# Optimization experiments

Measured on AMD Instinct MI355X. Metric: run time of the kernel, lower is better.

The kernel has to match this reference:

```python
import jax, jax.numpy as jnp
import numpy as np

B, V, H = 4, 256, 128
EPS = 1e-5


def setup_inputs() -> dict:
    key = jax.random.key(0)
    ks = jax.random.split(key, 16)
    inp = {
        "h1": jax.random.normal(ks[0], (B, V, H), jnp.float32),
        "h2": jax.random.normal(ks[1], (B, V, H), jnp.float32),
        "e": jax.random.normal(ks[2], (B, V, V, H), jnp.float32),
        "graph": jax.random.randint(ks[3], (B, V, V), 0, 2, jnp.int32),
    }
    scale = 1.0 / np.sqrt(H)
    for i, nm in enumerate(["U1", "U2", "V1", "V2", "A1", "A2", "C"]):
        inp[f"W_{nm}"] = jax.random.normal(ks[4 + i], (H, H), jnp.float32) * scale
        inp[f"b_{nm}"] = jnp.zeros((H,), jnp.float32)
    for nm in ["h1", "h2", "e"]:
        inp[f"g_{nm}"] = jnp.ones((H,), jnp.float32)   # BN gamma
        inp[f"be_{nm}"] = jnp.zeros((H,), jnp.float32)  # BN beta
    return inp


def _lin(x, W, b):
    # torch nn.Linear: x @ W.T + b
    return jnp.einsum('...i,oi->...o', x, W) + b


def _bn(x, g, b):
    # BatchNorm1d with track_running_stats=False: batch stats over flattened leading dims
    sh = x.shape
    x2 = x.reshape(-1, sh[-1])
    m = x2.mean(axis=0)
    v = x2.var(axis=0)  # biased, as torch BN uses for normalization
    return ((x2 - m) * jax.lax.rsqrt(v + EPS) * g + b).reshape(sh)


def reference(h1, h2, e, graph,
              W_U1, b_U1, W_U2, b_U2, W_V1, b_V1, W_V2, b_V2,
              W_A1, b_A1, W_A2, b_A2, W_C, b_C,
              g_h1, be_h1, g_h2, be_h2, g_e, be_e):
    h1_in, h2_in, e_in = h1, h2, e

    Uh1 = _lin(h1, W_U1, b_U1)
    Uh2 = _lin(h2, W_U2, b_U2)
    Vh1 = _lin(h1, W_V1, b_V1)
    Vh2 = _lin(h2, W_V2, b_V2)

    # Wh1[b,i,j,h] = Vh1[b,j,h] + Vh2[b,i,h] ; Wh2 = transpose(1,2) pattern
    Wh1 = Vh1[:, None, :, :] + Vh2[:, :, None, :]
    Wh2 = Vh1[:, :, None, :] + Vh2[:, None, :, :]

    Ah1 = _lin(h1, W_A1, b_A1)
    Ah2 = _lin(h2, W_A2, b_A2)
    Ce = _lin(e, W_C, b_C)
    e_new = Ah1[:, None, :, :] + Ah2[:, :, None, :] + Ce  # B x V x V x H

    gates = jax.nn.sigmoid(e_new)
    gates_T = jax.nn.sigmoid(jnp.transpose(e_new, (0, 2, 1, 3)))

    # aggregation = 'sum' over dim 2 (graph unused for sum)
    h1n = Uh1 + jnp.sum(gates * Wh1, axis=2)
    h2n = Uh2 + jnp.sum(gates_T * Wh2, axis=2)

    h1n = jax.nn.relu(_bn(h1n, g_h1, be_h1))
    h2n = jax.nn.relu(_bn(h2n, g_h2, be_h2))
    e_out = jax.nn.relu(_bn(e_new, g_e, be_e))

    # mode == 'residual'
    return (h1_in + h1n, h2_in + h2n, e_in + e_out)
```

## Files before the change

### kernel.cpp

```cpp
#include <hip/hip_runtime.h>
#include <math.h>

#define BB 4
#define VV 256
#define HH 128
#define EPS 1e-5f

typedef __attribute__((ext_vector_type(8))) short short8;
typedef __attribute__((ext_vector_type(8))) __bf16 bf16x8;
typedef __attribute__((ext_vector_type(4))) float f32x4;

__device__ __forceinline__ float sigm_(float x) {
    return 1.0f / (1.0f + __expf(-x));
}

__device__ __forceinline__ bf16x8 as_bf(short8 s) {
    union { short8 s; bf16x8 b; } u; u.s = s; return u.b;
}

__device__ __forceinline__ void split8(const float4 x0, const float4 x1,
                                       short8& hi, short8& lo) {
    float xs[8] = {x0.x, x0.y, x0.z, x0.w, x1.x, x1.y, x1.z, x1.w};
    #pragma unroll
    for (int i = 0; i < 8; ++i) {
        unsigned u = __float_as_uint(xs[i]);
        unsigned hr = (u + 0x7fffu + ((u >> 16) & 1u)) & 0xffff0000u;
        hi[i] = (short)(hr >> 16);
        float r = xs[i] - __uint_as_float(hr);
        lo[i] = (short)(__float_as_uint(r) >> 16);
    }
}

__global__ __launch_bounds__(256) void k0_splitW(const float* __restrict__ W_C,
                                                 short* __restrict__ Whl) {
    int t = blockIdx.x * 256 + threadIdx.x;
    int lane = t & 63;
    int grp = t >> 6;
    int kstep = grp >> 3, nsub = grp & 7;
    int n = nsub * 16 + (lane & 15);
    int kb = kstep * 32 + ((lane >> 4) & 3) * 8;
    const float4* src = (const float4*)(W_C + (size_t)n * HH + kb);
    float4 x0 = src[0], x1 = src[1];
    short8 hi, lo;
    split8(x0, x1, hi, lo);
    short8* dst = (short8*)Whl;
    dst[(grp * 2 + 0) * 64 + lane] = hi;
    dst[(grp * 2 + 1) * 64 + lane] = lo;
}

struct LinArgs {
    const float* x1; const float* x2;
    const float* W[6]; const float* b[6];
    float* out[6];
};

__global__ __launch_bounds__(128) void k1_linears(LinArgs a) {
    __shared__ float xs[2][8][HH];
    const int t = threadIdx.x;
    const int r0 = blockIdx.x * 8;
    {
        const float4* s1 = (const float4*)(a.x1 + (size_t)r0 * HH);
        const float4* s2 = (const float4*)(a.x2 + (size_t)r0 * HH);
        float4* d1 = (float4*)&xs[0][0][0];
        float4* d2 = (float4*)&xs[1][0][0];
        #pragma unroll
        for (int p = 0; p < 2; ++p) {
            d1[t + p * 128] = s1[t + p * 128];
            d2[t + p * 128] = s2[t + p * 128];
        }
    }
    __syncthreads();
    const int h = t;
    for (int g = 0; g < 6; ++g) {
        const float* W = a.W[g];
        const float (*x)[HH] = (g < 3) ? xs[0] : xs[1];
        float acc[8];
        #pragma unroll
        for (int r = 0; r < 8; ++r) acc[r] = 0.f;
        const float4* Wrow = (const float4*)(W + (size_t)h * HH);
        #pragma unroll 8
        for (int kq = 0; kq < 32; ++kq) {
            float4 w4 = Wrow[kq];
            #pragma unroll
            for (int r = 0; r < 8; ++r) {
                float4 ev = *(const float4*)&x[r][kq * 4];
                acc[r] = fmaf(ev.x, w4.x, acc[r]);
                acc[r] = fmaf(ev.y, w4.y, acc[r]);
                acc[r] = fmaf(ev.z, w4.z, acc[r]);
                acc[r] = fmaf(ev.w, w4.w, acc[r]);
            }
        }
        float bias = a.b[g][h];
        float* O = a.out[g] + (size_t)r0 * HH + h;
        #pragma unroll
        for (int r = 0; r < 8; ++r) O[(size_t)r * HH] = acc[r] + bias;
    }
}

__global__ __launch_bounds__(512) void k2_main(
    const float* __restrict__ e,
    const short* __restrict__ Whl,
    const float* __restrict__ b_C,
    const float* __restrict__ A1, const float* __restrict__ A2,
    const float* __restrict__ V1, const float* __restrict__ V2,
    const float* __restrict__ U1,
    float* __restrict__ e_new,
    float* __restrict__ h1p,
    float* __restrict__ stats)
{
    __shared__ float red[8][3][8][16];
    const int t = threadIdx.x;
    const int l = t & 63;
    const int w = t >> 6;
    const int l15 = l & 15;
    const int lq = (l >> 4) & 3;
    const int bi = blockIdx.x;
    const int b = bi >> 8;

    const float* ebase = e + (size_t)bi * (VV * HH);
    const short8* Wf = (const short8*)Whl;

    f32x4 acc[2][8];
    #pragma unroll
    for (int js = 0; js < 2; ++js)
        #pragma unroll
        for (int ns = 0; ns < 8; ++ns)
            acc[js][ns] = (f32x4){0.f, 0.f, 0.f, 0.f};

    for (int kstep = 0; kstep < 4; ++kstep) {
        short8 bh[8], bl[8];
        #pragma unroll
        for (int ns = 0; ns < 8; ++ns) {
            int grp = kstep * 8 + ns;
            bh[ns] = Wf[(grp * 2 + 0) * 64 + l];
            bl[ns] = Wf[(grp * 2 + 1) * 64 + l];
        }
        short8 ah[2], al[2];
        #pragma unroll
        for (int js = 0; js < 2; ++js) {
            int row = w * 32 + js * 16 + l15;
            const float4* p = (const float4*)(ebase + (size_t)row * HH +
                                              kstep * 32 + lq * 8);
            float4 x0 = p[0], x1 = p[1];
            split8(x0, x1, ah[js], al[js]);
        }
        #pragma unroll
        for (int ns = 0; ns < 8; ++ns) {
            #pragma unroll
            for (int js = 0; js < 2; ++js) {
                acc[js][ns] = __builtin_amdgcn_mfma_f32_16x16x32_bf16(
                    as_bf(ah[js]), as_bf(bh[ns]), acc[js][ns], 0, 0, 0);
                acc[js][ns] = __builtin_amdgcn_mfma_f32_16x16x32_bf16(
                    as_bf(ah[js]), as_bf(bl[ns]), acc[js][ns], 0, 0, 0);
                acc[js][ns] = __builtin_amdgcn_mfma_f32_16x16x32_bf16(
                    as_bf(al[js]), as_bf(bh[ns]), acc[js][ns], 0, 0, 0);
            }
        }
    }

    float bCv[8], ah2v[8], vh2v[8];
    #pragma unroll
    for (int ns = 0; ns < 8; ++ns) {
        int n = ns * 16 + l15;
        bCv[ns]  = b_C[n];
        ah2v[ns] = A2[(size_t)bi * HH + n];
        vh2v[ns] = V2[(size_t)bi * HH + n];
    }
    float h1a[8], es[8], eq[8];
    #pragma unroll
    for (int ns = 0; ns < 8; ++ns) { h1a[ns] = 0.f; es[ns] = 0.f; eq[ns] = 0.f; }

    #pragma unroll
    for (int js = 0; js < 2; ++js) {
        #pragma unroll
        for (int r = 0; r < 4; ++r) {
            int j = w * 32 + js * 16 + lq * 4 + r;
            size_t base = (size_t)(b * VV + j) * HH;
            size_t obase = ((size_t)bi * VV + j) * HH;
            #pragma unroll
            for (int ns = 0; ns < 8; ++ns) {
                int n = ns * 16 + l15;
                float en = acc[js][ns][r] + bCv[ns] + A1[base + n] + ah2v[ns];
                e_new[obase + n] = en;
                float s = sigm_(en);
                h1a[ns] = fmaf(s, V1[base + n] + vh2v[ns], h1a[ns]);
                es[ns] += en;
                eq[ns] = fmaf(en, en, eq[ns]);
            }
        }
    }

    #pragma unroll
    for (int ns = 0; ns < 8; ++ns) {
        h1a[ns] += __shfl_xor(h1a[ns], 16);
        h1a[ns] += __shfl_xor(h1a[ns], 32);
        es[ns]  += __shfl_xor(es[ns], 16);
        es[ns]  += __shfl_xor(es[ns], 32);
        eq[ns]  += __shfl_xor(eq[ns], 16);
        eq[ns]  += __shfl_xor(eq[ns], 32);
    }
    if (l < 16) {
        #pragma unroll
        for (int ns = 0; ns < 8; ++ns) {
            red[w][0][ns][l15] = h1a[ns];
            red[w][1][ns][l15] = es[ns];
            red[w][2][ns][l15] = eq[ns];
        }
    }
    __syncthreads();
    if (t < 128) {
        int ns = t >> 4, li = t & 15;
        float h1t = 0.f, est = 0.f, eqt = 0.f;
        #pragma unroll
        for (int ww = 0; ww < 8; ++ww) {
            h1t += red[ww][0][ns][li];
            est += red[ww][1][ns][li];
            eqt += red[ww][2][ns][li];
        }
        int n = t;
        float pre = U1[(size_t)bi * HH + n] + h1t;
        h1p[(size_t)bi * HH + n] = pre;
        atomicAdd(&stats[0 * HH + n], est);
        atomicAdd(&stats[1 * HH + n], eqt);
        atomicAdd(&stats[2 * HH + n], pre);
        atomicAdd(&stats[3 * HH + n], pre * pre);
    }
}

__global__ __launch_bounds__(256) void k4_pass2(
    float* __restrict__ e_io,
    const float* __restrict__ e_in,
    const float* __restrict__ V1, const float* __restrict__ V2,
    const float* __restrict__ U2,
    const float* __restrict__ g_e, const float* __restrict__ be_e,
    float* __restrict__ h2p,
    float* __restrict__ stats)
{
    const int t = threadIdx.x;
    const int h = t & 127;
    const int jsub = t >> 7;
    const int blk = blockIdx.x;
    const int b = blk >> 7;
    const int J0 = (blk & 127) << 1;
    const int J = J0 + jsub;
    const int bJ = (b << 8) + J;

    const float inv_n = 1.0f / (float)(BB * VV * VV);
    float mean = stats[0 * HH + h] * inv_n;
    float var  = stats[1 * HH + h] * inv_n - mean * mean;
    float rstd = rsqrtf(var + EPS);
    float sc = rstd * g_e[h];
    float sh = be_e[h] - mean * sc;

    const float vh1 = V1[(size_t)bJ * HH + h];
    float h2acc = 0.f;

    #pragma unroll 8
    for (int I = 0; I < VV; ++I) {
        size_t off = ((size_t)((b * VV + I) * VV) + J0) * HH + t;
        float en = e_io[off];
        float s = sigm_(en);
        h2acc = fmaf(s, vh1 + V2[(size_t)((b << 8) + I) * HH + h], h2acc);
        float bn = fmaf(en, sc, sh);
        e_io[off] = e_in[off] + fmaxf(bn, 0.f);
    }
    float pre = U2[(size_t)bJ * HH + h] + h2acc;
    h2p[(size_t)bJ * HH + h] = pre;
    atomicAdd(&stats[4 * HH + h], pre);
    atomicAdd(&stats[5 * HH + h], pre * pre);
}

__global__ __launch_bounds__(256) void k5_final(
    const float* __restrict__ h1_in, const float* __restrict__ h2_in,
    const float* __restrict__ h1p, const float* __restrict__ h2p,
    const float* __restrict__ g1, const float* __restrict__ be1,
    const float* __restrict__ g2, const float* __restrict__ be2,
    float* __restrict__ out,
    const float* __restrict__ stats)
{
    const float inv_n = 1.0f / 1024.0f;
    int idx0 = blockIdx.x * 2048 + threadIdx.x;
    #pragma unroll
    for (int p = 0; p < 8; ++p) {
        int idx = idx0 + p * 256;
        int region = idx >> 17;
        int local = idx & 131071;
        int h = idx & 127;
        float ssum = stats[(2 + 2 * region) * HH + h];
        float ssq  = stats[(3 + 2 * region) * HH + h];
        float mean = ssum * inv_n;
        float var  = ssq * inv_n - mean * mean;
        float rstd = rsqrtf(var + EPS);
        const float* g  = region ? g2 : g1;
        const float* be = region ? be2 : be1;
        float sc = rstd * g[h];
        float sh = be[h] - mean * sc;
        const float* xin = region ? h2_in : h1_in;
        const float* pre = region ? h2p : h1p;
        out[idx] = xin[local] + fmaxf(fmaf(pre[local], sc, sh), 0.f);
    }
}

extern "C" void kernel_launch(void* const* d_in, const int* in_sizes, int n_in,
                              void* d_out, int out_size, void* d_ws, size_t ws_size,
                              hipStream_t stream) {
    const float* h1   = (const float*)d_in[0];
    const float* h2   = (const float*)d_in[1];
    const float* e    = (const float*)d_in[2];
    const float* W_U1 = (const float*)d_in[4];
    const float* b_U1 = (const float*)d_in[5];
    const float* W_U2 = (const float*)d_in[6];
    const float* b_U2 = (const float*)d_in[7];
    const float* W_V1 = (const float*)d_in[8];
    const float* b_V1 = (const float*)d_in[9];
    const float* W_V2 = (const float*)d_in[10];
    const float* b_V2 = (const float*)d_in[11];
    const float* W_A1 = (const float*)d_in[12];
    const float* b_A1 = (const float*)d_in[13];
    const float* W_A2 = (const float*)d_in[14];
    const float* b_A2 = (const float*)d_in[15];
    const float* W_C  = (const float*)d_in[16];
    const float* b_C  = (const float*)d_in[17];
    const float* g_h1 = (const float*)d_in[18];
    const float* be_h1= (const float*)d_in[19];
    const float* g_h2 = (const float*)d_in[20];
    const float* be_h2= (const float*)d_in[21];
    const float* g_e  = (const float*)d_in[22];
    const float* be_e = (const float*)d_in[23];

    float* ws = (float*)d_ws;
    const int S = BB * VV * HH;
    float* U1 = ws + 0 * (size_t)S;
    float* U2 = ws + 1 * (size_t)S;
    float* V1 = ws + 2 * (size_t)S;
    float* V2 = ws + 3 * (size_t)S;
    float* A1 = ws + 4 * (size_t)S;
    float* A2 = ws + 5 * (size_t)S;
    float* h1p = ws + 6 * (size_t)S;
    float* h2p = ws + 7 * (size_t)S;
    float* stats = ws + 8 * (size_t)S;
    short* Whl  = (short*)(stats + 768);

    float* out = (float*)d_out;
    float* eo = out + 2 * (size_t)S;

    hipMemsetAsync(stats, 0, 6 * HH * sizeof(float), stream);

    k0_splitW<<<8, 256, 0, stream>>>(W_C, Whl);

    LinArgs la;
    la.x1 = h1; la.x2 = h2;
    la.W[0] = W_U1; la.b[0] = b_U1; la.out[0] = U1;
    la.W[1] = W_V1; la.b[1] = b_V1; la.out[1] = V1;
    la.W[2] = W_A1; la.b[2] = b_A1; la.out[2] = A1;
    la.W[3] = W_U2; la.b[3] = b_U2; la.out[3] = U2;
    la.W[4] = W_V2; la.b[4] = b_V2; la.out[4] = V2;
    la.W[5] = W_A2; la.b[5] = b_A2; la.out[5] = A2;
    k1_linears<<<128, 128, 0, stream>>>(la);

    k2_main<<<BB * VV, 512, 0, stream>>>(e, Whl, b_C, A1, A2, V1, V2, U1,
                                         eo, h1p, stats);

    k4_pass2<<<BB * VV / 2, 256, 0, stream>>>(eo, e, V1, V2, U2, g_e, be_e,
                                              h2p, stats);

    k5_final<<<128, 256, 0, stream>>>(h1, h2, h1p, h2p,
                                      g_h1, be_h1, g_h2, be_h2, out, stats);
}
```

Before: 221.4 us.

## Recompute edge GEMM in second pass instead of storing and rereading e_new

The first pass no longer writes the pre-BN edge tensor. It only accumulates the h1 aggregation and the BN statistics, using a grid with twice as many blocks, each covering half the j range. The second pass re-reads e, recomputes the W_C projection with split-bf16 MFMA and applies BN, ReLU and the residual directly. It also builds the h2 aggregation in tiled form through shared memory and atomics. The goal is to remove a full write plus re-read of the large edge intermediate, at the cost of a doubled MFMA GEMM, extra atomics and an added combine kernel; the bf16 split now uses native conversions.

```diff
diff --git a/kernel.cpp b/kernel.cpp
--- a/kernel.cpp
+++ b/kernel.cpp
@@ -18,16 +18,16 @@
     union { short8 s; bf16x8 b; } u; u.s = s; return u.b;
 }
 
-__device__ __forceinline__ void split8(const float4 x0, const float4 x1,
-                                       short8& hi, short8& lo) {
+__device__ __forceinline__ void split8n(const float4 x0, const float4 x1,
+                                        bf16x8& hi, bf16x8& lo) {
     float xs[8] = {x0.x, x0.y, x0.z, x0.w, x1.x, x1.y, x1.z, x1.w};
     #pragma unroll
     for (int i = 0; i < 8; ++i) {
-        unsigned u = __float_as_uint(xs[i]);
-        unsigned hr = (u + 0x7fffu + ((u >> 16) & 1u)) & 0xffff0000u;
-        hi[i] = (short)(hr >> 16);
-        float r = xs[i] - __uint_as_float(hr);
-        lo[i] = (short)(__float_as_uint(r) >> 16);
+        float x = xs[i];
+        __bf16 h = (__bf16)x;
+        float r = x - (float)h;
+        hi[i] = h;
+        lo[i] = (__bf16)r;
     }
 }
 
@@ -41,11 +41,13 @@
     int kb = kstep * 32 + ((lane >> 4) & 3) * 8;
     const float4* src = (const float4*)(W_C + (size_t)n * HH + kb);
     float4 x0 = src[0], x1 = src[1];
-    short8 hi, lo;
-    split8(x0, x1, hi, lo);
+    bf16x8 hi, lo;
+    split8n(x0, x1, hi, lo);
+    union { bf16x8 b; short8 s; } uh, ul;
+    uh.b = hi; ul.b = lo;
     short8* dst = (short8*)Whl;
-    dst[(grp * 2 + 0) * 64 + lane] = hi;
-    dst[(grp * 2 + 1) * 64 + lane] = lo;
+    dst[(grp * 2 + 0) * 64 + lane] = uh.s;
+    dst[(grp * 2 + 1) * 64 + lane] = ul.s;
 }
 
 struct LinArgs {
@@ -97,25 +99,26 @@
     }
 }
 
-__global__ __launch_bounds__(512) void k2_main(
+__global__ __launch_bounds__(256) void k2_pass1(
     const float* __restrict__ e,
     const short* __restrict__ Whl,
     const float* __restrict__ b_C,
     const float* __restrict__ A1, const float* __restrict__ A2,
     const float* __restrict__ V1, const float* __restrict__ V2,
-    const float* __restrict__ U1,
-    float* __restrict__ e_new,
-    float* __restrict__ h1p,
+    float* __restrict__ h1acc,
     float* __restrict__ stats)
 {
-    __shared__ float red[8][3][8][16];
+    __shared__ float red[4][3][8][16];
     const int t = threadIdx.x;
     const int l = t & 63;
     const int w = t >> 6;
     const int l15 = l & 15;
     const int lq = (l >> 4) & 3;
-    const int bi = blockIdx.x;
+    const int blk = blockIdx.x;
+    const int bi = blk >> 1;
+    const int jhalf = blk & 1;
     const int b = bi >> 8;
+    const int jbase = jhalf * 128 + w * 32;
 
     const float* ebase = e + (size_t)bi * (VV * HH);
     const short8* Wf = (const short8*)Whl;
@@ -135,25 +138,24 @@
             bh[ns] = Wf[(grp * 2 + 0) * 64 + l];
             bl[ns] = Wf[(grp * 2 + 1) * 64 + l];
         }
-        short8 ah[2], al[2];
+        bf16x8 ah[2], al[2];
         #pragma unroll
         for (int js = 0; js < 2; ++js) {
-            int row = w * 32 + js * 16 + l15;
+            int row = jbase + js * 16 + l15;
             const float4* p = (const float4*)(ebase + (size_t)row * HH +
                                               kstep * 32 + lq * 8);
-            float4 x0 = p[0], x1 = p[1];
-            split8(x0, x1, ah[js], al[js]);
+            split8n(p[0], p[1], ah[js], al[js]);
         }
         #pragma unroll
         for (int ns = 0; ns < 8; ++ns) {
             #pragma unroll
             for (int js = 0; js < 2; ++js) {
                 acc[js][ns] = __builtin_amdgcn_mfma_f32_16x16x32_bf16(
-                    as_bf(ah[js]), as_bf(bh[ns]), acc[js][ns], 0, 0, 0);
+                    ah[js], as_bf(bh[ns]), acc[js][ns], 0, 0, 0);
                 acc[js][ns] = __builtin_amdgcn_mfma_f32_16x16x32_bf16(
-                    as_bf(ah[js]), as_bf(bl[ns]), acc[js][ns], 0, 0, 0);
+                    ah[js], as_bf(bl[ns]), acc[js][ns], 0, 0, 0);
                 acc[js][ns] = __builtin_amdgcn_mfma_f32_16x16x32_bf16(
-                    as_bf(al[js]), as_bf(bh[ns]), acc[js][ns], 0, 0, 0);
+                    al[js], as_bf(bh[ns]), acc[js][ns], 0, 0, 0);
             }
         }
     }
@@ -174,14 +176,12 @@
     for (int js = 0; js < 2; ++js) {
         #pragma unroll
         for (int r = 0; r < 4; ++r) {
-            int j = w * 32 + js * 16 + lq * 4 + r;
+            int j = jbase + js * 16 + lq * 4 + r;
             size_t base = (size_t)(b * VV + j) * HH;
-            size_t obase = ((size_t)bi * VV + j) * HH;
             #pragma unroll
             for (int ns = 0; ns < 8; ++ns) {
                 int n = ns * 16 + l15;
                 float en = acc[js][ns][r] + bCv[ns] + A1[base + n] + ah2v[ns];
-                e_new[obase + n] = en;
                 float s = sigm_(en);
                 h1a[ns] = fmaf(s, V1[base + n] + vh2v[ns], h1a[ns]);
                 es[ns] += en;
@@ -212,62 +212,170 @@
         int ns = t >> 4, li = t & 15;
         float h1t = 0.f, est = 0.f, eqt = 0.f;
         #pragma unroll
-        for (int ww = 0; ww < 8; ++ww) {
+        for (int ww = 0; ww < 4; ++ww) {
             h1t += red[ww][0][ns][li];
             est += red[ww][1][ns][li];
             eqt += red[ww][2][ns][li];
         }
         int n = t;
-        float pre = U1[(size_t)bi * HH + n] + h1t;
-        h1p[(size_t)bi * HH + n] = pre;
+        atomicAdd(&h1acc[(size_t)bi * HH + n], h1t);
         atomicAdd(&stats[0 * HH + n], est);
         atomicAdd(&stats[1 * HH + n], eqt);
-        atomicAdd(&stats[2 * HH + n], pre);
-        atomicAdd(&stats[3 * HH + n], pre * pre);
     }
 }
 
 __global__ __launch_bounds__(256) void k4_pass2(
-    float* __restrict__ e_io,
-    const float* __restrict__ e_in,
+    const float* __restrict__ e,
+    const short* __restrict__ Whl,
+    const float* __restrict__ b_C,
+    const float* __restrict__ A1, const float* __restrict__ A2,
     const float* __restrict__ V1, const float* __restrict__ V2,
-    const float* __restrict__ U2,
     const float* __restrict__ g_e, const float* __restrict__ be_e,
-    float* __restrict__ h2p,
+    float* __restrict__ eo,
+    float* __restrict__ h2acc,
+    const float* __restrict__ stats)
+{
+    __shared__ float pre1[16][132];
+    __shared__ float v1s[16][132];
+    __shared__ float hacc[16][132];
+    const int t = threadIdx.x;
+    const int l = t & 63;
+    const int w = t >> 6;
+    const int l15 = l & 15;
+    const int lq = (l >> 4) & 3;
+    const int blk = blockIdx.x;
+    const int ic = blk & 15;
+    const int jt = (blk >> 4) & 15;
+    const int b = blk >> 8;
+    const int J0 = jt * 16;
+
+    #pragma unroll
+    for (int p = 0; p < 8; ++p) {
+        int idx = p * 256 + t;
+        int jj = idx >> 7, c = idx & 127;
+        size_t row = (size_t)(b * VV + J0 + jj) * HH + c;
+        pre1[jj][c] = A1[row] + b_C[c];
+        v1s[jj][c] = V1[row];
+        hacc[jj][c] = 0.f;
+    }
+    const float inv_n = 1.0f / (float)(BB * VV * VV);
+    float sc_r[8], sh_r[8];
+    #pragma unroll
+    for (int ns = 0; ns < 8; ++ns) {
+        int n = ns * 16 + l15;
+        float m = stats[0 * HH + n] * inv_n;
+        float v = stats[1 * HH + n] * inv_n - m * m;
+        float rs = rsqrtf(v + EPS);
+        sc_r[ns] = rs * g_e[n];
+        sh_r[ns] = be_e[n] - m * sc_r[ns];
+    }
+    __syncthreads();
+
+    const short8* Wf = (const short8*)Whl;
+    f32x4 h2a[8];
+    #pragma unroll
+    for (int ns = 0; ns < 8; ++ns) h2a[ns] = (f32x4){0.f, 0.f, 0.f, 0.f};
+
+    #pragma unroll
+    for (int u = 0; u < 4; ++u) {
+        const int I = ic * 16 + w * 4 + u;
+        const size_t rbase = ((size_t)(b * VV + I) * VV + J0) * HH;
+
+        f32x4 acc[8];
+        #pragma unroll
+        for (int ns = 0; ns < 8; ++ns) acc[ns] = (f32x4){0.f, 0.f, 0.f, 0.f};
+
+        for (int kstep = 0; kstep < 4; ++kstep) {
+            bf16x8 ah, al;
+            const float4* p = (const float4*)(e + rbase + (size_t)l15 * HH +
+                                              kstep * 32 + lq * 8);
+            split8n(p[0], p[1], ah, al);
+            #pragma unroll
+            for (int ns = 0; ns < 8; ++ns) {
+                int grp = kstep * 8 + ns;
+                short8 bh = Wf[(grp * 2 + 0) * 64 + l];
+                short8 bl = Wf[(grp * 2 + 1) * 64 + l];
+                acc[ns] = __builtin_amdgcn_mfma_f32_16x16x32_bf16(
+                    ah, as_bf(bh), acc[ns], 0, 0, 0);
+                acc[ns] = __builtin_amdgcn_mfma_f32_16x16x32_bf16(
+                    ah, as_bf(bl), acc[ns], 0, 0, 0);
+                acc[ns] = __builtin_amdgcn_mfma_f32_16x16x32_bf16(
+                    al, as_bf(bh), acc[ns], 0, 0, 0);
+            }
+        }
+
+        float a2v[8], v2v[8];
+        #pragma unroll
+        for (int ns = 0; ns < 8; ++ns) {
+            int n = ns * 16 + l15;
+            a2v[ns] = A2[(size_t)(b * VV + I) * HH + n];
+            v2v[ns] = V2[(size_t)(b * VV + I) * HH + n];
+        }
+        #pragma unroll
+        for (int ns = 0; ns < 8; ++ns) {
+            #pragma unroll
+            for (int r = 0; r < 4; ++r) {
+                int jj = lq * 4 + r;
+                int n = ns * 16 + l15;
+                float en = acc[ns][r] + pre1[jj][n] + a2v[ns];
+                size_t off = rbase + (size_t)jj * HH + n;
+                float bn = fmaf(en, sc_r[ns], sh_r[ns]);
+                eo[off] = e[off] + fmaxf(bn, 0.f);
+                float s = sigm_(en);
+                h2a[ns][r] = fmaf(s, v1s[jj][n] + v2v[ns], h2a[ns][r]);
+            }
+        }
+    }
+
+    for (int w2 = 0; w2 < 4; ++w2) {
+        if (w == w2) {
+            #pragma unroll
+            for (int ns = 0; ns < 8; ++ns)
+                #pragma unroll
+                for (int r = 0; r < 4; ++r)
+                    hacc[lq * 4 + r][ns * 16 + l15] += h2a[ns][r];
+        }
+        __syncthreads();
+    }
+    #pragma unroll
+    for (int p = 0; p < 8; ++p) {
+        int idx = p * 256 + t;
+        int jj = idx >> 7, c = idx & 127;
+        atomicAdd(&h2acc[(size_t)(b * VV + J0 + jj) * HH + c], hacc[jj][c]);
+    }
+}
+
+__global__ __launch_bounds__(256) void k45_combine(
+    const float* __restrict__ h1acc, const float* __restrict__ h2acc,
+    const float* __restrict__ U1, const float* __restrict__ U2,
+    float* __restrict__ h1p, float* __restrict__ h2p,
     float* __restrict__ stats)
 {
+    __shared__ float red[2][2][128];
     const int t = threadIdx.x;
     const int h = t & 127;
-    const int jsub = t >> 7;
-    const int blk = blockIdx.x;
-    const int b = blk >> 7;
-    const int J0 = (blk & 127) << 1;
-    const int J = J0 + jsub;
-    const int bJ = (b << 8) + J;
-
-    const float inv_n = 1.0f / (float)(BB * VV * VV);
-    float mean = stats[0 * HH + h] * inv_n;
-    float var  = stats[1 * HH + h] * inv_n - mean * mean;
-    float rstd = rsqrtf(var + EPS);
-    float sc = rstd * g_e[h];
-    float sh = be_e[h] - mean * sc;
-
-    const float vh1 = V1[(size_t)bJ * HH + h];
-    float h2acc = 0.f;
-
-    #pragma unroll 8
-    for (int I = 0; I < VV; ++I) {
-        size_t off = ((size_t)((b * VV + I) * VV) + J0) * HH + t;
-        float en = e_io[off];
-        float s = sigm_(en);
-        h2acc = fmaf(s, vh1 + V2[(size_t)((b << 8) + I) * HH + h], h2acc);
-        float bn = fmaf(en, sc, sh);
-        e_io[off] = e_in[off] + fmaxf(bn, 0.f);
-    }
-    float pre = U2[(size_t)bJ * HH + h] + h2acc;
-    h2p[(size_t)bJ * HH + h] = pre;
-    atomicAdd(&stats[4 * HH + h], pre);
-    atomicAdd(&stats[5 * HH + h], pre * pre);
+    const int rr = t >> 7;
+    const int region = blockIdx.x >> 5;
+    const int r0 = (blockIdx.x & 31) * 32;
+    const float* acc = region ? h2acc : h1acc;
+    const float* U   = region ? U2 : U1;
+    float* hp        = region ? h2p : h1p;
+    float s = 0.f, q = 0.f;
+    #pragma unroll
+    for (int rs = 0; rs < 16; ++rs) {
+        size_t idx = (size_t)(r0 + rr * 16 + rs) * HH + h;
+        float v = acc[idx] + U[idx];
+        hp[idx] = v;
+        s += v;
+        q = fmaf(v, v, q);
+    }
+    red[0][rr][h] = s;
+    red[1][rr][h] = q;
+    __syncthreads();
+    if (t < 128) {
+        atomicAdd(&stats[(2 + 2 * region) * HH + h], red[0][0][h] + red[0][1][h]);
+        atomicAdd(&stats[(3 + 2 * region) * HH + h], red[1][0][h] + red[1][1][h]);
+    }
 }
 
 __global__ __launch_bounds__(256) void k5_final(
@@ -329,22 +437,24 @@
     const float* be_e = (const float*)d_in[23];
 
     float* ws = (float*)d_ws;
-    const int S = BB * VV * HH;
-    float* U1 = ws + 0 * (size_t)S;
-    float* U2 = ws + 1 * (size_t)S;
-    float* V1 = ws + 2 * (size_t)S;
-    float* V2 = ws + 3 * (size_t)S;
-    float* A1 = ws + 4 * (size_t)S;
-    float* A2 = ws + 5 * (size_t)S;
-    float* h1p = ws + 6 * (size_t)S;
-    float* h2p = ws + 7 * (size_t)S;
-    float* stats = ws + 8 * (size_t)S;
+    const size_t S = (size_t)BB * VV * HH;
+    float* U1 = ws + 0 * S;
+    float* U2 = ws + 1 * S;
+    float* V1 = ws + 2 * S;
+    float* V2 = ws + 3 * S;
+    float* A1 = ws + 4 * S;
+    float* A2 = ws + 5 * S;
+    float* h1p = ws + 6 * S;
+    float* h2p = ws + 7 * S;
+    float* h1acc = ws + 8 * S;
+    float* h2acc = ws + 9 * S;
+    float* stats = ws + 10 * S;
     short* Whl  = (short*)(stats + 768);
 
     float* out = (float*)d_out;
-    float* eo = out + 2 * (size_t)S;
-
-    hipMemsetAsync(stats, 0, 6 * HH * sizeof(float), stream);
+    float* eo = out + 2 * S;
+
+    hipMemsetAsync(h1acc, 0, (2 * S + 768) * sizeof(float), stream);
 
     k0_splitW<<<8, 256, 0, stream>>>(W_C, Whl);
 
@@ -358,11 +468,13 @@
     la.W[5] = W_A2; la.b[5] = b_A2; la.out[5] = A2;
     k1_linears<<<128, 128, 0, stream>>>(la);
 
-    k2_main<<<BB * VV, 512, 0, stream>>>(e, Whl, b_C, A1, A2, V1, V2, U1,
-                                         eo, h1p, stats);
-
-    k4_pass2<<<BB * VV / 2, 256, 0, stream>>>(eo, e, V1, V2, U2, g_e, be_e,
-                                              h2p, stats);
+    k2_pass1<<<BB * VV * 2, 256, 0, stream>>>(e, Whl, b_C, A1, A2, V1, V2,
+                                              h1acc, stats);
+
+    k4_pass2<<<BB * 16 * 16, 256, 0, stream>>>(e, Whl, b_C, A1, A2, V1, V2,
+                                               g_e, be_e, eo, h2acc, stats);
+
+    k45_combine<<<64, 256, 0, stream>>>(h1acc, h2acc, U1, U2, h1p, h2p, stats);
 
     k5_final<<<128, 256, 0, stream>>>(h1, h2, h1p, h2p,
                                       g_h1, be_h1, g_h2, be_h2, out, stats);
```

New measurement: 313.1 us. 1.41x slower.
